# Kernel optimization log

Hardware: AMD Instinct MI355X
Metric: run time of the kernel (lower is better)

The kernel has to match this reference:

```python
import jax, jax.numpy as jnp
import numpy as np

B, C, T = 8, 256, 2048
DS = 4
SC = C // DS          # tsa_scale = 64
DEPTH = 256           # temporal_depth (band width)
BN_EPS = 1e-5


def _conv_bn_relu(x, W, b, g, beta, mu, var):
    # 1x1 conv on [B, C, T, 1] layout == channel matmul, then eval-mode BN, then ReLU
    y = jnp.einsum('bctz,oc->botz', x, W) + b[None, :, None, None]
    inv = g / jnp.sqrt(var + BN_EPS)
    y = (y - mu[None, :, None, None]) * inv[None, :, None, None] + beta[None, :, None, None]
    return jax.nn.relu(y)


def setup_inputs() -> dict:
    key = jax.random.key(0)
    ks = jax.random.split(key, 20)
    inp = {"x": jax.random.normal(ks[0], (B, C, T, 1), jnp.float32)}
    for name, oc, base in (("k", SC, 1), ("q", SC, 7), ("v", C, 13)):
        inp[name + "W"] = jax.random.normal(ks[base], (oc, C), jnp.float32) * 0.05
        inp[name + "b"] = jax.random.normal(ks[base + 1], (oc,), jnp.float32) * 0.05
        inp[name + "g"] = 1.0 + 0.05 * jax.random.normal(ks[base + 2], (oc,), jnp.float32)
        inp[name + "beta"] = jax.random.normal(ks[base + 3], (oc,), jnp.float32) * 0.05
        inp[name + "mu"] = jax.random.normal(ks[base + 4], (oc,), jnp.float32) * 0.05
        inp[name + "var"] = 1.0 + 0.1 * jax.random.uniform(ks[base + 5], (oc,), jnp.float32)
    return inp


def reference(x, kW, kb, kg, kbeta, kmu, kvar,
              qW, qb, qg, qbeta, qmu, qvar,
              vW, vb, vg, vbeta, vmu, vvar):
    key = _conv_bn_relu(x, kW, kb, kg, kbeta, kmu, kvar)[..., 0]                      # [B, SC, T]
    query = _conv_bn_relu(x, qW, qb, qg, qbeta, qmu, qvar)[..., 0].transpose(0, 2, 1)  # [B, T, SC]
    value = _conv_bn_relu(x, vW, vb, vg, vbeta, vmu, vvar)[..., 0].transpose(0, 2, 1)  # [B, T, C]

    i = jnp.arange(T)
    # tril(diag=0) * triu(diag=-(DEPTH-1)): causal band of width DEPTH
    mask = ((i[:, None] >= i[None, :]) & (i[:, None] - i[None, :] <= DEPTH - 1)).astype(x.dtype)

    s = jnp.einsum('btd,bds->bts', query, key) * mask / np.float32(np.sqrt(SC))
    s = jnp.exp(s - jnp.max(s, axis=2, keepdims=True)) * mask
    # NOTE: original torch code does `torch.sum(...)[0]`, indexing batch 0 of the
    # sum tensor ([T,1]) and broadcasting it across the batch. Replicated faithfully.
    s = s / (jnp.sum(s, axis=2, keepdims=True)[0] + 1e-30)

    tsa_out = jnp.einsum('bts,bsc->btc', s, value)                                     # [B, T, C]
    return x + tsa_out.transpose(0, 2, 1)[..., None]                                   # res_skip
```

## Files before the change

### kernel.cpp

```cpp
#include <hip/hip_runtime.h>

#define TDIM 2048

typedef __bf16 bf16_t;
typedef bf16_t bf16x8 __attribute__((ext_vector_type(8)));
typedef float f32x4 __attribute__((ext_vector_type(4)));
typedef unsigned short us8 __attribute__((ext_vector_type(8)));

__device__ __forceinline__ unsigned short f2bf(float x) {
  unsigned u = __builtin_bit_cast(unsigned, x);
  u += 0x7fffu + ((u >> 16) & 1u);
  return (unsigned short)(u >> 16);
}

__device__ __forceinline__ void gl_lds16(const unsigned short* g, unsigned short* l) {
  __builtin_amdgcn_global_load_lds(
      (const __attribute__((address_space(1))) unsigned int*)g,
      (__attribute__((address_space(3))) unsigned int*)l, 16, 0, 0);
}

__global__ __launch_bounds__(256) void k_prepw(
    const float* __restrict__ kW, const float* __restrict__ kb,
    const float* __restrict__ kg, const float* __restrict__ kbe,
    const float* __restrict__ kmu, const float* __restrict__ kva,
    const float* __restrict__ qW, const float* __restrict__ qb,
    const float* __restrict__ qg, const float* __restrict__ qbe,
    const float* __restrict__ qmu, const float* __restrict__ qva,
    const float* __restrict__ vW, const float* __restrict__ vb,
    const float* __restrict__ vg, const float* __restrict__ vbe,
    const float* __restrict__ vmu, const float* __restrict__ vva,
    unsigned short* __restrict__ effWf,
    float* __restrict__ effb)
{
  const int idx = blockIdx.x;
  const int tid = threadIdx.x;
  const int gid = idx >> 2, cc = idx & 3;
  unsigned short* dst = effWf + (size_t)idx * 8192;
#pragma unroll
  for (int pass = 0; pass < 4; ++pass) {
    int f = pass * 256 + tid;
    int ocblk = f >> 7, cblk = (f >> 4) & 7, m = f & 15;
    int G = gid * 128 + ocblk * 16 + m;
    const float* Wp = (G < 64) ? (kW + G * 256)
                     : (G < 128) ? (qW + (G - 64) * 256)
                                 : (vW + (G - 128) * 256);
    float gg = (G < 64) ? kg[G]  : (G < 128) ? qg[G - 64]  : vg[G - 128];
    float vr = (G < 64) ? kva[G] : (G < 128) ? qva[G - 64] : vva[G - 128];
    float inv = gg * rsqrtf(vr + 1e-5f);
    int c = cc * 64 + cblk * 8;
    float4 a = *(const float4*)(Wp + c);
    float4 bq = *(const float4*)(Wp + c + 4);
    ushort4 lo, hi;
    lo.x = f2bf(a.x * inv);  lo.y = f2bf(a.y * inv);
    lo.z = f2bf(a.z * inv);  lo.w = f2bf(a.w * inv);
    hi.x = f2bf(bq.x * inv); hi.y = f2bf(bq.y * inv);
    hi.z = f2bf(bq.z * inv); hi.w = f2bf(bq.w * inv);
    *(ushort4*)(dst + f * 8) = lo;
    *(ushort4*)(dst + f * 8 + 4) = hi;
  }
  if (idx == 0) {
    for (int G = tid; G < 384; G += 256) {
      float gg = (G < 64) ? kg[G]  : (G < 128) ? qg[G - 64]  : vg[G - 128];
      float vr = (G < 64) ? kva[G] : (G < 128) ? qva[G - 64] : vva[G - 128];
      float bb = (G < 64) ? kb[G]  : (G < 128) ? qb[G - 64]  : vb[G - 128];
      float mm = (G < 64) ? kmu[G] : (G < 128) ? qmu[G - 64] : vmu[G - 128];
      float be = (G < 64) ? kbe[G] : (G < 128) ? qbe[G - 64] : vbe[G - 128];
      float inv = gg * rsqrtf(vr + 1e-5f);
      effb[G] = (bb - mm) * inv + be;
    }
  }
}

__global__ __launch_bounds__(256, 3) void k_qkv(
    const unsigned short* __restrict__ effWf,
    const float* __restrict__ effb,
    const float* __restrict__ x,
    unsigned short* __restrict__ vv,
    unsigned short* __restrict__ kTs,
    unsigned short* __restrict__ qTs)
{
  const int tb = blockIdx.x, gid = blockIdx.y, b = blockIdx.z;
  const int tid = threadIdx.x;
  const int lane = tid & 63, wv = tid >> 6;
  const int m = lane & 15, quad = lane >> 4;
  const int t0 = tb * 64;

  __shared__ unsigned short Wb[2][8192];
  __shared__ unsigned short Xs[4608];
  __shared__ float effbs[128];

  if (tid < 128) effbs[tid] = effb[gid * 128 + tid];

  const unsigned short* wbase = effWf + (size_t)gid * 32768;
  const float* xb = x + (size_t)b * 256 * TDIM + t0 + lane;

  float xr[16];

  auto stageW = [&](int cc, int bufi) {
    const unsigned short* ws = wbase + cc * 8192;
#pragma unroll
    for (int i = 0; i < 4; ++i) {
      int ii = wv * 4 + i;
      gl_lds16(ws + (ii * 64 + lane) * 8, &Wb[bufi][ii * 512]);
    }
  };
  auto loadX = [&](int cc) {
#pragma unroll
    for (int p = 0; p < 4; ++p)
#pragma unroll
      for (int j = 0; j < 4; ++j) {
        int c = cc * 64 + p * 16 + wv * 4 + j;
        xr[p * 4 + j] = xb[(size_t)c * TDIM];
      }
  };

  const f32x4 fz = {0.f, 0.f, 0.f, 0.f};
  f32x4 acc[2][4];
#pragma unroll
  for (int i = 0; i < 2; ++i)
#pragma unroll
    for (int j = 0; j < 4; ++j) acc[i][j] = fz;

  stageW(0, 0);
  loadX(0);
  for (int cc = 0; cc < 4; ++cc) {
    __syncthreads();
#pragma unroll
    for (int p = 0; p < 4; ++p) {
      int cb4 = p * 16 + wv * 4;
      int swz = (((cb4 >> 3) ^ (lane >> 3)) << 3) | (cb4 & 7);
      ushort4 s4;
      s4.x = f2bf(xr[p * 4 + 0]); s4.y = f2bf(xr[p * 4 + 1]);
      s4.z = f2bf(xr[p * 4 + 2]); s4.w = f2bf(xr[p * 4 + 3]);
      *(ushort4*)&Xs[lane * 72 + swz] = s4;
    }
    if (cc < 3) { stageW(cc + 1, (cc + 1) & 1); loadX(cc + 1); }
    __syncthreads();
    const unsigned short* Wc = Wb[cc & 1];
#pragma unroll
    for (int kk = 0; kk < 2; ++kk) {
      int cb = kk * 4 + quad;
      bf16x8 af[2], bfv[4];
#pragma unroll
      for (int mt = 0; mt < 2; ++mt)
        af[mt] = *(const bf16x8*)&Wc[(((wv * 2 + mt) * 8 + cb) * 16 + m) * 8];
#pragma unroll
      for (int nt = 0; nt < 4; ++nt) {
        int t = nt * 16 + m;
        bfv[nt] = *(const bf16x8*)&Xs[t * 72 + ((cb ^ (t >> 3)) << 3)];
      }
#pragma unroll
      for (int mt = 0; mt < 2; ++mt)
#pragma unroll
        for (int nt = 0; nt < 4; ++nt)
          acc[mt][nt] = __builtin_amdgcn_mfma_f32_16x16x32_bf16(af[mt], bfv[nt], acc[mt][nt], 0, 0, 0);
    }
  }

  if (gid == 0) {
#pragma unroll
    for (int mt = 0; mt < 2; ++mt)
#pragma unroll
      for (int nt = 0; nt < 4; ++nt) {
        int ocl = wv * 32 + mt * 16 + quad * 4;
        int t = t0 + nt * 16 + m;
        ushort4 s4;
        s4.x = f2bf(fmaxf(acc[mt][nt][0] + effbs[ocl + 0], 0.f));
        s4.y = f2bf(fmaxf(acc[mt][nt][1] + effbs[ocl + 1], 0.f));
        s4.z = f2bf(fmaxf(acc[mt][nt][2] + effbs[ocl + 2], 0.f));
        s4.w = f2bf(fmaxf(acc[mt][nt][3] + effbs[ocl + 3], 0.f));
        if (ocl < 64) {
          int col = (((ocl >> 3) ^ (t & 7)) << 3) | (ocl & 7);
          *(ushort4*)(kTs + ((size_t)(b * TDIM + t)) * 64 + col) = s4;
        } else {
          int oq = ocl - 64;
          int col = (((oq >> 3) ^ (t & 7)) << 3) | (oq & 7);
          *(ushort4*)(qTs + ((size_t)(b * TDIM + t)) * 64 + col) = s4;
        }
      }
  } else {
#pragma unroll
    for (int mt = 0; mt < 2; ++mt)
#pragma unroll
      for (int nt = 0; nt < 4; ++nt)
#pragma unroll
        for (int r = 0; r < 4; ++r) {
          int ocl = wv * 32 + mt * 16 + quad * 4 + r;
          float y = fmaxf(acc[mt][nt][r] + effbs[ocl], 0.f);
          int c = (gid - 1) * 128 + ocl;
          int t = t0 + nt * 16 + m;
          vv[(size_t)(b * 256 + c) * TDIM + t] = f2bf(y);
        }
  }
}

__global__ __launch_bounds__(512, 1) void k_denom(
    const unsigned short* __restrict__ kTs,
    const unsigned short* __restrict__ qTs,
    float* __restrict__ denom0)
{
  const int t0d = blockIdx.x * 16;
  const int tid = threadIdx.x;
  const int lane = tid & 63, w = tid >> 6;
  const int m = lane & 15, quad = lane >> 4;

  __shared__ unsigned short S[18432];
  unsigned short* Qs = S;
  unsigned short* Ks = S + 1024;
  __shared__ float pmaxs[8][16];
  __shared__ float psums[8][16];

  {
    const unsigned short* qg = qTs + (size_t)t0d * 64;
    const unsigned short* kg = kTs + ((long)t0d - 256) * 64;
#pragma unroll
    for (int it = 0; it < 5; ++it) {
      int j = it * 512 + tid;
      if (j < 2304) {
        const unsigned short* g = (j < 128) ? (qg + j * 8) : (kg + (size_t)(j - 128) * 8);
        gl_lds16(g, &S[(it * 512 + w * 64) * 8]);
      }
    }
  }
  __syncthreads();

  const int jn = (w == 0) ? 3 : 2;
  f32x4 sc[3];
  {
    int t = m;
    bf16x8 qf0 = *(const bf16x8*)&Qs[t * 64 + ((quad ^ (t & 7)) << 3)];
    bf16x8 qf1 = *(const bf16x8*)&Qs[t * 64 + (((4 + quad) ^ (t & 7)) << 3)];
    const f32x4 fz = {0.f, 0.f, 0.f, 0.f};
#pragma unroll
    for (int jj = 0; jj < 3; ++jj) {
      if (jj < jn) {
        int j = w + jj * 8;
        int sr = 16 * j + m;
        f32x4 a = fz;
        bf16x8 kf0 = *(const bf16x8*)&Ks[sr * 64 + ((quad ^ (sr & 7)) << 3)];
        a = __builtin_amdgcn_mfma_f32_16x16x32_bf16(qf0, kf0, a, 0, 0, 0);
        bf16x8 kf1 = *(const bf16x8*)&Ks[sr * 64 + (((4 + quad) ^ (sr & 7)) << 3)];
        a = __builtin_amdgcn_mfma_f32_16x16x32_bf16(qf1, kf1, a, 0, 0, 0);
        sc[jj] = a;
      }
    }
  }

  float mx[4] = {0.f, 0.f, 0.f, 0.f};
#pragma unroll
  for (int jj = 0; jj < 3; ++jj)
    if (jj < jn) {
      int j = w + jj * 8;
#pragma unroll
      for (int r = 0; r < 4; ++r) {
        float v = sc[jj][r] * 0.125f;
        sc[jj][r] = v;
        int tg = t0d + quad * 4 + r;
        int sg = t0d - 256 + 16 * j + m;
        if (sg >= 0 && sg <= tg && tg - sg < 256) mx[r] = fmaxf(mx[r], v);
      }
    }
#pragma unroll
  for (int d = 1; d < 16; d <<= 1)
#pragma unroll
    for (int r = 0; r < 4; ++r) mx[r] = fmaxf(mx[r], __shfl_xor(mx[r], d, 64));
  if (m == 0)
#pragma unroll
    for (int r = 0; r < 4; ++r) pmaxs[w][quad * 4 + r] = mx[r];
  __syncthreads();

  float mxf[4];
#pragma unroll
  for (int r = 0; r < 4; ++r) {
    float v = pmaxs[0][quad * 4 + r];
#pragma unroll
    for (int ww = 1; ww < 8; ++ww) v = fmaxf(v, pmaxs[ww][quad * 4 + r]);
    mxf[r] = v;
  }
  float sm[4] = {0.f, 0.f, 0.f, 0.f};
#pragma unroll
  for (int jj = 0; jj < 3; ++jj)
    if (jj < jn) {
      int j = w + jj * 8;
#pragma unroll
      for (int r = 0; r < 4; ++r) {
        int tg = t0d + quad * 4 + r;
        int sg = t0d - 256 + 16 * j + m;
        if (sg >= 0 && sg <= tg && tg - sg < 256) sm[r] += __expf(sc[jj][r] - mxf[r]);
      }
    }
#pragma unroll
  for (int d = 1; d < 16; d <<= 1)
#pragma unroll
    for (int r = 0; r < 4; ++r) sm[r] += __shfl_xor(sm[r], d, 64);
  if (m == 0)
#pragma unroll
    for (int r = 0; r < 4; ++r) psums[w][quad * 4 + r] = sm[r];
  __syncthreads();

  if (tid < 16) {
    float s = 0.f;
#pragma unroll
    for (int ww = 0; ww < 8; ++ww) s += psums[ww][tid];
    denom0[t0d + tid] = s;
  }
}

__global__ __launch_bounds__(512, 2) void k_attn(
    const float* __restrict__ x,
    const unsigned short* __restrict__ vv,
    const unsigned short* __restrict__ kTs,
    const unsigned short* __restrict__ qTs,
    const float* __restrict__ denom0,
    float* __restrict__ out)
{
  const int bx = blockIdx.x, b = blockIdx.y;
  const int tb = (bx >> 3) + 4 * (bx & 7);
  const int tid = threadIdx.x;
  const int lane = tid & 63, w = tid >> 6;
  const int m = lane & 15, quad = lane >> 4;
  const int t0 = tb * 64;

  __shared__ unsigned short SM[24576];
  __shared__ float pmaxs[128];
  unsigned short* Qs = SM;
  unsigned short* Ks = SM + 4096;
  unsigned short* Ps = SM;

  {
    const unsigned short* qg = qTs + ((size_t)(b * TDIM + t0)) * 64;
    const unsigned short* kg = kTs + ((long)(b * TDIM + t0) - 256) * 64;
#pragma unroll
    for (int it = 0; it < 6; ++it) {
      int j = it * 512 + tid;
      const unsigned short* g = (j < 512) ? (qg + (size_t)j * 8)
                                          : (kg + (size_t)(j - 512) * 8);
      gl_lds16(g, &SM[(it * 512 + w * 64) * 8]);
    }
  }
  const int rt = w & 3, half = w >> 2;
  const int tw = t0 + rt * 16;
  float dval[4];
#pragma unroll
  for (int r = 0; r < 4; ++r) dval[r] = denom0[tw + quad * 4 + r];
  __syncthreads();

  const int j0 = half ? 9 : 0;
  const int jn = half ? 8 : 9;
  f32x4 sc[9];
  {
    int t = rt * 16 + m;
    bf16x8 qf0 = *(const bf16x8*)&Qs[t * 64 + ((quad ^ (t & 7)) << 3)];
    bf16x8 qf1 = *(const bf16x8*)&Qs[t * 64 + (((4 + quad) ^ (t & 7)) << 3)];
    const f32x4 fz = {0.f, 0.f, 0.f, 0.f};
#pragma unroll
    for (int jj = 0; jj < 9; ++jj) {
      if (jj < jn) {
        int sr = 16 * (rt + j0 + jj) + m;
        f32x4 a = fz;
        bf16x8 kf0 = *(const bf16x8*)&Ks[sr * 64 + ((quad ^ (sr & 7)) << 3)];
        a = __builtin_amdgcn_mfma_f32_16x16x32_bf16(qf0, kf0, a, 0, 0, 0);
        bf16x8 kf1 = *(const bf16x8*)&Ks[sr * 64 + (((4 + quad) ^ (sr & 7)) << 3)];
        a = __builtin_amdgcn_mfma_f32_16x16x32_bf16(qf1, kf1, a, 0, 0, 0);
        sc[jj] = a;
      }
    }
  }

  float mx[4] = {0.f, 0.f, 0.f, 0.f};
#pragma unroll
  for (int jj = 0; jj < 9; ++jj)
    if (jj < jn) {
#pragma unroll
      for (int r = 0; r < 4; ++r) {
        float v = sc[jj][r] * 0.125f;
        sc[jj][r] = v;
        int tg = tw + quad * 4 + r;
        int sg = t0 - 256 + 16 * (rt + j0 + jj) + m;
        if (sg >= 0 && sg <= tg && tg - sg < 256) mx[r] = fmaxf(mx[r], v);
      }
    }
#pragma unroll
  for (int d = 1; d < 16; d <<= 1)
#pragma unroll
    for (int r = 0; r < 4; ++r) mx[r] = fmaxf(mx[r], __shfl_xor(mx[r], d, 64));
  if (m == 0)
#pragma unroll
    for (int r = 0; r < 4; ++r) pmaxs[half * 64 + rt * 16 + quad * 4 + r] = mx[r];

  __syncthreads();

  float mxf[4], rden[4];
#pragma unroll
  for (int r = 0; r < 4; ++r) {
    int row = rt * 16 + quad * 4 + r;
    mxf[r] = fmaxf(pmaxs[row], pmaxs[64 + row]);
    rden[r] = 1.f / (dval[r] + 1e-30f);
  }
#pragma unroll
  for (int jj = 0; jj < 9; ++jj)
    if (jj < jn) {
#pragma unroll
      for (int r = 0; r < 4; ++r) {
        int tg = tw + quad * 4 + r;
        int sg = t0 - 256 + 16 * (rt + j0 + jj) + m;
        bool ib = (sg >= 0 && sg <= tg && tg - sg < 256);
        sc[jj][r] = ib ? __expf(sc[jj][r] - mxf[r]) * rden[r] : 0.f;
      }
    }

  if (half == 0) {
    if (rt > 0) {
      int row = rt * 16 + (lane >> 2), col = 16 * rt - 16 + (lane & 3) * 4;
      ushort4 z; z.x = 0; z.y = 0; z.z = 0; z.w = 0;
      *(ushort4*)&Ps[row * 344 + col] = z;
    }
  } else {
    if (rt < 3) {
      int row = rt * 16 + (lane >> 2), col = 16 * rt + 272 + (lane & 3) * 4;
      ushort4 z; z.x = 0; z.y = 0; z.z = 0; z.w = 0;
      *(ushort4*)&Ps[row * 344 + col] = z;
    }
  }
#pragma unroll
  for (int jj = 0; jj < 9; ++jj)
    if (jj < jn) {
      int col = 16 * (rt + j0 + jj) + m;
#pragma unroll
      for (int r = 0; r < 4; ++r)
        Ps[(rt * 16 + quad * 4 + r) * 344 + col] = f2bf(sc[jj][r]);
    }

  const int cbase = w * 32;
  const unsigned short* vrow0 = vv + (size_t)(b * 256 + cbase + m) * TDIM;
  const unsigned short* vrow1 = vrow0 + (size_t)16 * TDIM;
  us8 vreg0 = {0, 0, 0, 0, 0, 0, 0, 0}, vreg1 = {0, 0, 0, 0, 0, 0, 0, 0};
  if (t0 >= 256) {
    vreg0 = *(const us8*)(vrow0 + t0 - 256 + quad * 8);
    vreg1 = *(const us8*)(vrow1 + t0 - 256 + quad * 8);
  }

  __syncthreads();

  float4 xv[4][2];
#pragma unroll
  for (int mt = 0; mt < 4; ++mt)
#pragma unroll
    for (int ct = 0; ct < 2; ++ct) {
      int c = cbase + ct * 16 + m;
      int t = t0 + mt * 16 + quad * 4;
      xv[mt][ct] = *(const float4*)(x + (size_t)(b * 256 + c) * TDIM + t);
    }

  const f32x4 fz = {0.f, 0.f, 0.f, 0.f};
  f32x4 acc[4][2];
#pragma unroll
  for (int i = 0; i < 4; ++i) { acc[i][0] = fz; acc[i][1] = fz; }
#pragma unroll
  for (int chunk = 0; chunk < 10; ++chunk) {
    us8 vn0 = {0, 0, 0, 0, 0, 0, 0, 0}, vn1 = {0, 0, 0, 0, 0, 0, 0, 0};
    if (chunk < 9) {
      int sbase = t0 - 256 + (chunk + 1) * 32;
      if (sbase >= 0) {
        vn0 = *(const us8*)(vrow0 + sbase + quad * 8);
        vn1 = *(const us8*)(vrow1 + sbase + quad * 8);
      }
    }
    bf16x8 bfr0 = __builtin_bit_cast(bf16x8, vreg0);
    bf16x8 bfr1 = __builtin_bit_cast(bf16x8, vreg1);
#pragma unroll
    for (int mt = 0; mt < 4; ++mt) {
      const int cs = mt >> 1;
      if (chunk >= cs && chunk <= cs + 8) {
        bf16x8 af = *(const bf16x8*)&Ps[(mt * 16 + m) * 344 + chunk * 32 + quad * 8];
        acc[mt][0] = __builtin_amdgcn_mfma_f32_16x16x32_bf16(af, bfr0, acc[mt][0], 0, 0, 0);
        acc[mt][1] = __builtin_amdgcn_mfma_f32_16x16x32_bf16(af, bfr1, acc[mt][1], 0, 0, 0);
      }
    }
    vreg0 = vn0; vreg1 = vn1;
  }

#pragma unroll
  for (int mt = 0; mt < 4; ++mt)
#pragma unroll
    for (int ct = 0; ct < 2; ++ct) {
      int c = cbase + ct * 16 + m;
      int t = t0 + mt * 16 + quad * 4;
      size_t off = (size_t)(b * 256 + c) * TDIM + t;
      float4 o;
      o.x = xv[mt][ct].x + acc[mt][ct][0];
      o.y = xv[mt][ct].y + acc[mt][ct][1];
      o.z = xv[mt][ct].z + acc[mt][ct][2];
      o.w = xv[mt][ct].w + acc[mt][ct][3];
      *(float4*)(out + off) = o;
    }
}

extern "C" void kernel_launch(void* const* d_in, const int* in_sizes, int n_in,
                              void* d_out, int out_size, void* d_ws, size_t ws_size,
                              hipStream_t stream) {
  const float* x   = (const float*)d_in[0];
  const float* kW  = (const float*)d_in[1];
  const float* kb  = (const float*)d_in[2];
  const float* kg  = (const float*)d_in[3];
  const float* kbe = (const float*)d_in[4];
  const float* kmu = (const float*)d_in[5];
  const float* kva = (const float*)d_in[6];
  const float* qW  = (const float*)d_in[7];
  const float* qb  = (const float*)d_in[8];
  const float* qg  = (const float*)d_in[9];
  const float* qbe = (const float*)d_in[10];
  const float* qmu = (const float*)d_in[11];
  const float* qva = (const float*)d_in[12];
  const float* vW  = (const float*)d_in[13];
  const float* vb  = (const float*)d_in[14];
  const float* vg  = (const float*)d_in[15];
  const float* vbe = (const float*)d_in[16];
  const float* vmu = (const float*)d_in[17];
  const float* vva = (const float*)d_in[18];

  unsigned short* vv  = (unsigned short*)d_ws;
  unsigned short* kTs = vv + (size_t)8 * 256 * TDIM;
  unsigned short* qTs = kTs + (size_t)8 * TDIM * 64;
  float* denom0 = (float*)(qTs + (size_t)8 * TDIM * 64);
  unsigned short* effWf = (unsigned short*)(denom0 + 2048);
  float* effb = (float*)(effWf + 12 * 8192);
  float* outp = (float*)d_out;

  k_prepw<<<dim3(12), 256, 0, stream>>>(
      kW, kb, kg, kbe, kmu, kva,
      qW, qb, qg, qbe, qmu, qva,
      vW, vb, vg, vbe, vmu, vva, effWf, effb);
  k_qkv<<<dim3(32, 3, 8), 256, 0, stream>>>(effWf, effb, x, vv, kTs, qTs);
  k_denom<<<dim3(128), 512, 0, stream>>>(kTs, qTs, denom0);
  k_attn<<<dim3(32, 8), 512, 0, stream>>>(x, vv, kTs, qTs, denom0, outp);
}
```

Baseline: 132.3 us.

## Merge QKV projection groups per block and shrink attention tiles to 32 rows

The QKV projection kernel now computes all 384 output channels in one 512-thread block per time tile. This loads and converts x to bf16 once instead of three times, and weights are read straight into registers instead of being staged in LDS. The attention kernel switches to 32-query tiles with 256 threads and 64 channels per wave. That doubles the block count, trims the wasted band-edge work in the PV loop (9 chunks instead of 10), and interleaves key tiles between waves. The cost is more register pressure per thread and more global weight traffic from registers, with K/V rows re-read across more blocks.

```diff
diff --git a/kernel.cpp b/kernel.cpp
--- a/kernel.cpp
+++ b/kernel.cpp
@@ -71,7 +71,7 @@
   }
 }
 
-__global__ __launch_bounds__(256, 3) void k_qkv(
+__global__ __launch_bounds__(512, 2) void k_qkv(
     const unsigned short* __restrict__ effWf,
     const float* __restrict__ effb,
     const float* __restrict__ x,
@@ -79,118 +79,122 @@
     unsigned short* __restrict__ kTs,
     unsigned short* __restrict__ qTs)
 {
-  const int tb = blockIdx.x, gid = blockIdx.y, b = blockIdx.z;
+  const int tb = blockIdx.x, b = blockIdx.y;
   const int tid = threadIdx.x;
   const int lane = tid & 63, wv = tid >> 6;
   const int m = lane & 15, quad = lane >> 4;
   const int t0 = tb * 64;
 
-  __shared__ unsigned short Wb[2][8192];
-  __shared__ unsigned short Xs[4608];
-  __shared__ float effbs[128];
-
-  if (tid < 128) effbs[tid] = effb[gid * 128 + tid];
-
-  const unsigned short* wbase = effWf + (size_t)gid * 32768;
+  __shared__ unsigned short Xs[64 * 72];
+  __shared__ float effbs[384];
+
+  if (tid < 384) effbs[tid] = effb[tid];
+
   const float* xb = x + (size_t)b * 256 * TDIM + t0 + lane;
-
-  float xr[16];
-
-  auto stageW = [&](int cc, int bufi) {
-    const unsigned short* ws = wbase + cc * 8192;
-#pragma unroll
-    for (int i = 0; i < 4; ++i) {
-      int ii = wv * 4 + i;
-      gl_lds16(ws + (ii * 64 + lane) * 8, &Wb[bufi][ii * 512]);
-    }
+  float xr[8];
+
+  auto loadX = [&](int cc) {
+#pragma unroll
+    for (int p = 0; p < 2; ++p)
+#pragma unroll
+      for (int j = 0; j < 4; ++j) {
+        int c = cc * 64 + p * 32 + wv * 4 + j;
+        xr[p * 4 + j] = xb[(size_t)c * TDIM];
+      }
   };
-  auto loadX = [&](int cc) {
-#pragma unroll
-    for (int p = 0; p < 4; ++p)
-#pragma unroll
-      for (int j = 0; j < 4; ++j) {
-        int c = cc * 64 + p * 16 + wv * 4 + j;
-        xr[p * 4 + j] = xb[(size_t)c * TDIM];
-      }
+  auto loadW = [&](bf16x8 (&dst)[2][3], int cc) {
+#pragma unroll
+    for (int kk = 0; kk < 2; ++kk) {
+      int cb = kk * 4 + quad;
+#pragma unroll
+      for (int mt = 0; mt < 3; ++mt) {
+        int T = wv * 3 + mt;
+        int gid = T >> 3, ocb = T & 7;
+        dst[kk][mt] = *(const bf16x8*)&effWf[
+            ((size_t)((gid * 4 + cc) * 1024) + ocb * 128 + cb * 16 + m) * 8];
+      }
+    }
   };
 
   const f32x4 fz = {0.f, 0.f, 0.f, 0.f};
-  f32x4 acc[2][4];
-#pragma unroll
-  for (int i = 0; i < 2; ++i)
+  f32x4 acc[3][4];
+#pragma unroll
+  for (int i = 0; i < 3; ++i)
 #pragma unroll
     for (int j = 0; j < 4; ++j) acc[i][j] = fz;
 
-  stageW(0, 0);
+  bf16x8 afn[2][3];
+  loadW(afn, 0);
   loadX(0);
+#pragma unroll
   for (int cc = 0; cc < 4; ++cc) {
     __syncthreads();
 #pragma unroll
-    for (int p = 0; p < 4; ++p) {
-      int cb4 = p * 16 + wv * 4;
+    for (int p = 0; p < 2; ++p) {
+      int cb4 = p * 32 + wv * 4;
       int swz = (((cb4 >> 3) ^ (lane >> 3)) << 3) | (cb4 & 7);
       ushort4 s4;
       s4.x = f2bf(xr[p * 4 + 0]); s4.y = f2bf(xr[p * 4 + 1]);
       s4.z = f2bf(xr[p * 4 + 2]); s4.w = f2bf(xr[p * 4 + 3]);
       *(ushort4*)&Xs[lane * 72 + swz] = s4;
     }
-    if (cc < 3) { stageW(cc + 1, (cc + 1) & 1); loadX(cc + 1); }
+    if (cc < 3) loadX(cc + 1);
+    bf16x8 afc[2][3];
+#pragma unroll
+    for (int kk = 0; kk < 2; ++kk)
+#pragma unroll
+      for (int mt = 0; mt < 3; ++mt) afc[kk][mt] = afn[kk][mt];
+    if (cc < 3) loadW(afn, cc + 1);
     __syncthreads();
-    const unsigned short* Wc = Wb[cc & 1];
 #pragma unroll
     for (int kk = 0; kk < 2; ++kk) {
       int cb = kk * 4 + quad;
-      bf16x8 af[2], bfv[4];
-#pragma unroll
-      for (int mt = 0; mt < 2; ++mt)
-        af[mt] = *(const bf16x8*)&Wc[(((wv * 2 + mt) * 8 + cb) * 16 + m) * 8];
+      bf16x8 bfv[4];
 #pragma unroll
       for (int nt = 0; nt < 4; ++nt) {
         int t = nt * 16 + m;
         bfv[nt] = *(const bf16x8*)&Xs[t * 72 + ((cb ^ (t >> 3)) << 3)];
       }
 #pragma unroll
-      for (int mt = 0; mt < 2; ++mt)
+      for (int mt = 0; mt < 3; ++mt)
 #pragma unroll
         for (int nt = 0; nt < 4; ++nt)
-          acc[mt][nt] = __builtin_amdgcn_mfma_f32_16x16x32_bf16(af[mt], bfv[nt], acc[mt][nt], 0, 0, 0);
-    }
-  }
-
-  if (gid == 0) {
-#pragma unroll
-    for (int mt = 0; mt < 2; ++mt)
-#pragma unroll
-      for (int nt = 0; nt < 4; ++nt) {
-        int ocl = wv * 32 + mt * 16 + quad * 4;
-        int t = t0 + nt * 16 + m;
+          acc[mt][nt] = __builtin_amdgcn_mfma_f32_16x16x32_bf16(
+              afc[kk][mt], bfv[nt], acc[mt][nt], 0, 0, 0);
+    }
+  }
+
+#pragma unroll
+  for (int mt = 0; mt < 3; ++mt) {
+    int T = wv * 3 + mt;
+    int ocg = T * 16 + quad * 4;
+#pragma unroll
+    for (int nt = 0; nt < 4; ++nt) {
+      int t = t0 + nt * 16 + m;
+      float ys[4];
+#pragma unroll
+      for (int r = 0; r < 4; ++r)
+        ys[r] = fmaxf(acc[mt][nt][r] + effbs[ocg + r], 0.f);
+      if (T < 8) {
         ushort4 s4;
-        s4.x = f2bf(fmaxf(acc[mt][nt][0] + effbs[ocl + 0], 0.f));
-        s4.y = f2bf(fmaxf(acc[mt][nt][1] + effbs[ocl + 1], 0.f));
-        s4.z = f2bf(fmaxf(acc[mt][nt][2] + effbs[ocl + 2], 0.f));
-        s4.w = f2bf(fmaxf(acc[mt][nt][3] + effbs[ocl + 3], 0.f));
-        if (ocl < 64) {
+        s4.x = f2bf(ys[0]); s4.y = f2bf(ys[1]);
+        s4.z = f2bf(ys[2]); s4.w = f2bf(ys[3]);
+        if (T < 4) {
+          int ocl = ocg;
           int col = (((ocl >> 3) ^ (t & 7)) << 3) | (ocl & 7);
           *(ushort4*)(kTs + ((size_t)(b * TDIM + t)) * 64 + col) = s4;
         } else {
-          int oq = ocl - 64;
+          int oq = ocg - 64;
           int col = (((oq >> 3) ^ (t & 7)) << 3) | (oq & 7);
           *(ushort4*)(qTs + ((size_t)(b * TDIM + t)) * 64 + col) = s4;
         }
-      }
-  } else {
-#pragma unroll
-    for (int mt = 0; mt < 2; ++mt)
-#pragma unroll
-      for (int nt = 0; nt < 4; ++nt)
-#pragma unroll
-        for (int r = 0; r < 4; ++r) {
-          int ocl = wv * 32 + mt * 16 + quad * 4 + r;
-          float y = fmaxf(acc[mt][nt][r] + effbs[ocl], 0.f);
-          int c = (gid - 1) * 128 + ocl;
-          int t = t0 + nt * 16 + m;
-          vv[(size_t)(b * 256 + c) * TDIM + t] = f2bf(y);
-        }
+      } else {
+        int c = ocg - 128;
+#pragma unroll
+        for (int r = 0; r < 4; ++r)
+          vv[(size_t)(b * 256 + c + r) * TDIM + t] = f2bf(ys[r]);
+      }
+    }
   }
 }
 
@@ -306,7 +310,7 @@
   }
 }
 
-__global__ __launch_bounds__(512, 2) void k_attn(
+__global__ __launch_bounds__(256, 2) void k_attn(
     const float* __restrict__ x,
     const unsigned short* __restrict__ vv,
     const unsigned short* __restrict__ kTs,
@@ -315,38 +319,36 @@
     float* __restrict__ out)
 {
   const int bx = blockIdx.x, b = blockIdx.y;
-  const int tb = (bx >> 3) + 4 * (bx & 7);
+  const int tb = (bx >> 3) + 8 * (bx & 7);
   const int tid = threadIdx.x;
   const int lane = tid & 63, w = tid >> 6;
   const int m = lane & 15, quad = lane >> 4;
-  const int t0 = tb * 64;
-
-  __shared__ unsigned short SM[24576];
-  __shared__ float pmaxs[128];
+  const int t0 = tb * 32;
+
+  __shared__ unsigned short SM[20480];
+  __shared__ float pmaxs[4][16];
   unsigned short* Qs = SM;
-  unsigned short* Ks = SM + 4096;
+  unsigned short* Ks = SM + 2048;
   unsigned short* Ps = SM;
 
   {
     const unsigned short* qg = qTs + ((size_t)(b * TDIM + t0)) * 64;
     const unsigned short* kg = kTs + ((long)(b * TDIM + t0) - 256) * 64;
 #pragma unroll
-    for (int it = 0; it < 6; ++it) {
-      int j = it * 512 + tid;
-      const unsigned short* g = (j < 512) ? (qg + (size_t)j * 8)
-                                          : (kg + (size_t)(j - 512) * 8);
-      gl_lds16(g, &SM[(it * 512 + w * 64) * 8]);
-    }
-  }
-  const int rt = w & 3, half = w >> 2;
-  const int tw = t0 + rt * 16;
+    for (int it = 0; it < 10; ++it) {
+      int j = it * 256 + tid;
+      const unsigned short* g = (j < 256) ? (qg + (size_t)j * 8)
+                                          : (kg + (size_t)(j - 256) * 8);
+      gl_lds16(g, &SM[(it * 256 + w * 64) * 8]);
+    }
+  }
+  const int rt = w & 1, jb = w >> 1;
+  const int jn = jb ? 8 : 9;
   float dval[4];
 #pragma unroll
-  for (int r = 0; r < 4; ++r) dval[r] = denom0[tw + quad * 4 + r];
+  for (int r = 0; r < 4; ++r) dval[r] = denom0[t0 + rt * 16 + quad * 4 + r];
   __syncthreads();
 
-  const int j0 = half ? 9 : 0;
-  const int jn = half ? 8 : 9;
   f32x4 sc[9];
   {
     int t = rt * 16 + m;
@@ -356,7 +358,8 @@
 #pragma unroll
     for (int jj = 0; jj < 9; ++jj) {
       if (jj < jn) {
-        int sr = 16 * (rt + j0 + jj) + m;
+        int js = rt + jb + 2 * jj;
+        int sr = 16 * js + m;
         f32x4 a = fz;
         bf16x8 kf0 = *(const bf16x8*)&Ks[sr * 64 + ((quad ^ (sr & 7)) << 3)];
         a = __builtin_amdgcn_mfma_f32_16x16x32_bf16(qf0, kf0, a, 0, 0, 0);
@@ -371,12 +374,13 @@
 #pragma unroll
   for (int jj = 0; jj < 9; ++jj)
     if (jj < jn) {
+      int js = rt + jb + 2 * jj;
 #pragma unroll
       for (int r = 0; r < 4; ++r) {
         float v = sc[jj][r] * 0.125f;
         sc[jj][r] = v;
-        int tg = tw + quad * 4 + r;
-        int sg = t0 - 256 + 16 * (rt + j0 + jj) + m;
+        int tg = t0 + rt * 16 + quad * 4 + r;
+        int sg = t0 - 256 + 16 * js + m;
         if (sg >= 0 && sg <= tg && tg - sg < 256) mx[r] = fmaxf(mx[r], v);
       }
     }
@@ -386,104 +390,107 @@
     for (int r = 0; r < 4; ++r) mx[r] = fmaxf(mx[r], __shfl_xor(mx[r], d, 64));
   if (m == 0)
 #pragma unroll
-    for (int r = 0; r < 4; ++r) pmaxs[half * 64 + rt * 16 + quad * 4 + r] = mx[r];
+    for (int r = 0; r < 4; ++r) pmaxs[w][quad * 4 + r] = mx[r];
 
   __syncthreads();
 
   float mxf[4], rden[4];
 #pragma unroll
   for (int r = 0; r < 4; ++r) {
-    int row = rt * 16 + quad * 4 + r;
-    mxf[r] = fmaxf(pmaxs[row], pmaxs[64 + row]);
+    mxf[r] = fmaxf(pmaxs[rt][quad * 4 + r], pmaxs[rt + 2][quad * 4 + r]);
     rden[r] = 1.f / (dval[r] + 1e-30f);
   }
 #pragma unroll
   for (int jj = 0; jj < 9; ++jj)
     if (jj < jn) {
+      int js = rt + jb + 2 * jj;
 #pragma unroll
       for (int r = 0; r < 4; ++r) {
-        int tg = tw + quad * 4 + r;
-        int sg = t0 - 256 + 16 * (rt + j0 + jj) + m;
+        int tg = t0 + rt * 16 + quad * 4 + r;
+        int sg = t0 - 256 + 16 * js + m;
         bool ib = (sg >= 0 && sg <= tg && tg - sg < 256);
         sc[jj][r] = ib ? __expf(sc[jj][r] - mxf[r]) * rden[r] : 0.f;
       }
     }
 
-  if (half == 0) {
-    if (rt > 0) {
-      int row = rt * 16 + (lane >> 2), col = 16 * rt - 16 + (lane & 3) * 4;
-      ushort4 z; z.x = 0; z.y = 0; z.z = 0; z.w = 0;
-      *(ushort4*)&Ps[row * 344 + col] = z;
-    }
-  } else {
-    if (rt < 3) {
-      int row = rt * 16 + (lane >> 2), col = 16 * rt + 272 + (lane & 3) * 4;
-      ushort4 z; z.x = 0; z.y = 0; z.z = 0; z.w = 0;
-      *(ushort4*)&Ps[row * 344 + col] = z;
-    }
+  if (jb == 0) {
+    int row = rt * 16 + (lane >> 2);
+    int col = (rt ? 0 : 272) + (lane & 3) * 4;
+    ushort4 z; z.x = 0; z.y = 0; z.z = 0; z.w = 0;
+    *(ushort4*)&Ps[row * 296 + col] = z;
   }
 #pragma unroll
   for (int jj = 0; jj < 9; ++jj)
     if (jj < jn) {
-      int col = 16 * (rt + j0 + jj) + m;
+      int js = rt + jb + 2 * jj;
+      int col = 16 * js + m;
 #pragma unroll
       for (int r = 0; r < 4; ++r)
-        Ps[(rt * 16 + quad * 4 + r) * 344 + col] = f2bf(sc[jj][r]);
-    }
-
-  const int cbase = w * 32;
-  const unsigned short* vrow0 = vv + (size_t)(b * 256 + cbase + m) * TDIM;
-  const unsigned short* vrow1 = vrow0 + (size_t)16 * TDIM;
-  us8 vreg0 = {0, 0, 0, 0, 0, 0, 0, 0}, vreg1 = {0, 0, 0, 0, 0, 0, 0, 0};
+        Ps[(rt * 16 + quad * 4 + r) * 296 + col] = f2bf(sc[jj][r]);
+    }
+
+  const int cbase = w * 64;
+  const us8 z8 = {0, 0, 0, 0, 0, 0, 0, 0};
+  const unsigned short* vrow[4];
+  us8 vreg[4];
+#pragma unroll
+  for (int ct = 0; ct < 4; ++ct) {
+    vrow[ct] = vv + (size_t)(b * 256 + cbase + ct * 16 + m) * TDIM;
+    vreg[ct] = z8;
+  }
   if (t0 >= 256) {
-    vreg0 = *(const us8*)(vrow0 + t0 - 256 + quad * 8);
-    vreg1 = *(const us8*)(vrow1 + t0 - 256 + quad * 8);
+#pragma unroll
+    for (int ct = 0; ct < 4; ++ct)
+      vreg[ct] = *(const us8*)(vrow[ct] + t0 - 256 + quad * 8);
   }
 
   __syncthreads();
 
-  float4 xv[4][2];
-#pragma unroll
-  for (int mt = 0; mt < 4; ++mt)
-#pragma unroll
-    for (int ct = 0; ct < 2; ++ct) {
+  float4 xv[2][4];
+#pragma unroll
+  for (int mt = 0; mt < 2; ++mt)
+#pragma unroll
+    for (int ct = 0; ct < 4; ++ct) {
       int c = cbase + ct * 16 + m;
       int t = t0 + mt * 16 + quad * 4;
       xv[mt][ct] = *(const float4*)(x + (size_t)(b * 256 + c) * TDIM + t);
     }
 
   const f32x4 fz = {0.f, 0.f, 0.f, 0.f};
-  f32x4 acc[4][2];
-#pragma unroll
-  for (int i = 0; i < 4; ++i) { acc[i][0] = fz; acc[i][1] = fz; }
-#pragma unroll
-  for (int chunk = 0; chunk < 10; ++chunk) {
-    us8 vn0 = {0, 0, 0, 0, 0, 0, 0, 0}, vn1 = {0, 0, 0, 0, 0, 0, 0, 0};
-    if (chunk < 9) {
+  f32x4 acc[2][4];
+#pragma unroll
+  for (int i = 0; i < 2; ++i)
+#pragma unroll
+    for (int j = 0; j < 4; ++j) acc[i][j] = fz;
+#pragma unroll
+  for (int chunk = 0; chunk < 9; ++chunk) {
+    us8 vn[4];
+#pragma unroll
+    for (int ct = 0; ct < 4; ++ct) vn[ct] = z8;
+    if (chunk < 8) {
       int sbase = t0 - 256 + (chunk + 1) * 32;
       if (sbase >= 0) {
-        vn0 = *(const us8*)(vrow0 + sbase + quad * 8);
-        vn1 = *(const us8*)(vrow1 + sbase + quad * 8);
-      }
-    }
-    bf16x8 bfr0 = __builtin_bit_cast(bf16x8, vreg0);
-    bf16x8 bfr1 = __builtin_bit_cast(bf16x8, vreg1);
-#pragma unroll
-    for (int mt = 0; mt < 4; ++mt) {
-      const int cs = mt >> 1;
-      if (chunk >= cs && chunk <= cs + 8) {
-        bf16x8 af = *(const bf16x8*)&Ps[(mt * 16 + m) * 344 + chunk * 32 + quad * 8];
-        acc[mt][0] = __builtin_amdgcn_mfma_f32_16x16x32_bf16(af, bfr0, acc[mt][0], 0, 0, 0);
-        acc[mt][1] = __builtin_amdgcn_mfma_f32_16x16x32_bf16(af, bfr1, acc[mt][1], 0, 0, 0);
-      }
-    }
-    vreg0 = vn0; vreg1 = vn1;
-  }
-
-#pragma unroll
-  for (int mt = 0; mt < 4; ++mt)
-#pragma unroll
-    for (int ct = 0; ct < 2; ++ct) {
+#pragma unroll
+        for (int ct = 0; ct < 4; ++ct)
+          vn[ct] = *(const us8*)(vrow[ct] + sbase + quad * 8);
+      }
+    }
+#pragma unroll
+    for (int mt = 0; mt < 2; ++mt) {
+      bf16x8 af = *(const bf16x8*)&Ps[(mt * 16 + m) * 296 + chunk * 32 + quad * 8];
+#pragma unroll
+      for (int ct = 0; ct < 4; ++ct)
+        acc[mt][ct] = __builtin_amdgcn_mfma_f32_16x16x32_bf16(
+            af, __builtin_bit_cast(bf16x8, vreg[ct]), acc[mt][ct], 0, 0, 0);
+    }
+#pragma unroll
+    for (int ct = 0; ct < 4; ++ct) vreg[ct] = vn[ct];
+  }
+
+#pragma unroll
+  for (int mt = 0; mt < 2; ++mt)
+#pragma unroll
+    for (int ct = 0; ct < 4; ++ct) {
       int c = cbase + ct * 16 + m;
       int t = t0 + mt * 16 + quad * 4;
       size_t off = (size_t)(b * 256 + c) * TDIM + t;
@@ -531,7 +538,7 @@
       kW, kb, kg, kbe, kmu, kva,
       qW, qb, qg, qbe, qmu, qva,
       vW, vb, vg, vbe, vmu, vva, effWf, effb);
-  k_qkv<<<dim3(32, 3, 8), 256, 0, stream>>>(effWf, effb, x, vv, kTs, qTs);
+  k_qkv<<<dim3(32, 8), 512, 0, stream>>>(effWf, effb, x, vv, kTs, qTs);
   k_denom<<<dim3(128), 512, 0, stream>>>(kTs, qTs, denom0);
-  k_attn<<<dim3(32, 8), 512, 0, stream>>>(x, vv, kTs, qTs, denom0, outp);
-}
+  k_attn<<<dim3(64, 8), 256, 0, stream>>>(x, vv, kTs, qTs, denom0, outp);
+}
```

Result: no change. 131.8 us (-0.4%).
